# Kernel optimization log

Hardware: AMD Instinct MI355X
Metric: run time of the kernel (lower is better)

Reference implementation:

```python
import jax, jax.numpy as jnp
import numpy as np

N_NODES = 40000
N_EDGES = 640000
D = 64          # node feature dim / out_features
HEADS = 4
K2 = 64         # n_grid_K**3
BN_EPS = 1e-5
SEG_EPS = 1e-16
R_EPS = 1e-8


def segment_softmax(alpha, seg, num_segments):
    # alpha: [E, H], seg: [E] int
    seg_max = jax.ops.segment_max(alpha, seg, num_segments=num_segments)
    seg_max = jnp.where(jnp.isfinite(seg_max), seg_max, 0.0)
    a = jnp.exp(alpha - seg_max[seg])
    denom = jax.ops.segment_sum(a, seg, num_segments=num_segments)
    return a / (denom[seg] + SEG_EPS)


def setup_inputs() -> dict:
    key = jax.random.key(0)
    ks = jax.random.split(key, 12)
    inp = {}
    inp["input"] = jax.random.normal(ks[0], (N_NODES, D), dtype=jnp.float32)
    inp["rij"] = jax.random.uniform(ks[1], (N_EDGES,), dtype=jnp.float32)
    inp["plane_wave"] = jax.random.normal(ks[2], (N_EDGES, K2), dtype=jnp.float32)
    inp["edge_attr"] = jax.random.normal(ks[3], (N_EDGES, D), dtype=jnp.float32)
    # learned parameters (torch Linear(in,out,bias=False) -> [in,out] here)
    def glorot(k, shape):
        fan = shape[0] + shape[-1]
        s = jnp.sqrt(6.0 / fan)
        return jax.random.uniform(k, shape, minval=-s, maxval=s, dtype=jnp.float32)
    inp["Wg"] = glorot(ks[4], (3 * D, D))          # linear_gate 192->64
    inp["Wm"] = glorot(ks[5], (3 * D, D))          # linear_MLP 192->64
    inp["W2"] = glorot(ks[6], (K2, D))             # linear2_vector
    inp["W2g"] = glorot(ks[7], (K2, K2))           # linear2_vector_gate
    inp["Wa"] = glorot(ks[8], (2 * D, HEADS * D))  # AGAT W
    inp["att"] = glorot(ks[9], (1, HEADS, 2 * D))  # AGAT att
    inp["bn_gamma"] = jnp.ones((HEADS,), dtype=jnp.float32)
    inp["bn_beta"] = jnp.zeros((HEADS,), dtype=jnp.float32)
    # graph indices
    src = jax.random.randint(ks[10], (N_EDGES,), 0, N_NODES, dtype=jnp.int32)
    tgt = jax.random.randint(ks[11], (N_EDGES,), 0, N_NODES, dtype=jnp.int32)
    inp["edge_sources"] = src
    inp["edge_targets"] = tgt
    inp["edge_index"] = jnp.stack([src, tgt], axis=0)
    inp["nodes"] = jnp.zeros((1,), dtype=jnp.int32)  # unused in forward
    return inp


def reference(input, rij, plane_wave, edge_attr, Wg, Wm, W2, W2g, Wa, att,
              bn_gamma, bn_beta, nodes, edge_sources, edge_targets, edge_index):
    # gated edge MLP branch
    ni = input[edge_sources]                       # [E, D]
    nj = input[edge_targets]                       # [E, D]
    r = rij + (rij == 0).astype(rij.dtype) * R_EPS
    delta = (ni - nj) / r[:, None]
    final_fe = jnp.concatenate([ni, nj, delta], axis=1)   # [E, 3D]
    e_gate = jax.nn.sigmoid(final_fe @ Wg)                 # [E, D]
    e_mlp = jax.nn.elu(final_fe @ Wm)                      # [E, D]
    # plane-wave gated linear branch
    gate = jax.nn.sigmoid(plane_wave @ W2g)                # [E, K2]
    z2 = (plane_wave * gate) @ W2                          # [E, D]
    # AGAT branch (eval-mode BatchNorm1d: running mean 0, var 1)
    row, col = edge_index[0], edge_index[1]
    out_i = jax.nn.softplus(jnp.concatenate([input[row], edge_attr], axis=1) @ Wa)
    out_j = jax.nn.softplus(jnp.concatenate([input[col], edge_attr], axis=1) @ Wa)
    out_i = out_i.reshape(-1, HEADS, D)                    # [E, H, D]
    out_j = out_j.reshape(-1, HEADS, D)
    alpha = jax.nn.softplus((jnp.concatenate([out_i, out_j], axis=-1) * att).sum(-1))  # [E, H]
    alpha = jax.nn.softplus(alpha / jnp.sqrt(1.0 + BN_EPS) * bn_gamma + bn_beta)
    alpha = segment_softmax(alpha, row, N_NODES)
    z1 = (out_j * alpha[:, :, None]).mean(axis=1)          # mean over heads -> [E, D]
    # combine + scatter-add
    z = e_gate * e_mlp * (z1 + z2)
    output = input.at[edge_sources].add(z)
    return output
```

## Files before the change

kernel.cpp:

```cpp
#include <hip/hip_runtime.h>
#include <math.h>

#define N_NODES 40000
#define N_EDGES 640000
#define NT0 16

typedef short short8 __attribute__((ext_vector_type(8)));
typedef unsigned short ushort8v __attribute__((ext_vector_type(8)));
typedef unsigned short ushort4v __attribute__((ext_vector_type(4)));
typedef float fragC __attribute__((ext_vector_type(4)));

__device__ __forceinline__ float softplus_f(float x) {
    return x > 15.f ? x : __logf(1.f + __expf(x));
}
__device__ __forceinline__ float sigmoid_f(float x) {
    return 1.f / (1.f + __expf(-x));
}
__device__ __forceinline__ short f2bf(float f) {
    unsigned u = __float_as_uint(f);
    u += 0x7FFF + ((u >> 16) & 1);
    return (short)(u >> 16);
}
__device__ __forceinline__ float bf2f(unsigned short u) {
    return __uint_as_float(((unsigned)u) << 16);
}

__global__ void k_weights(const float* __restrict__ Wa, const float* __restrict__ W2g,
                          const float* __restrict__ W2, short* __restrict__ WaTb,
                          short* __restrict__ W2gTb, short* __restrict__ W2Tb) {
    int idx = blockIdx.x * blockDim.x + threadIdx.x;
    int stride = gridDim.x * blockDim.x;
    for (int i = idx; i < 256 * 64; i += stride) {
        int c = i >> 6, k = i & 63;
        WaTb[i] = f2bf(Wa[(64 + k) * 256 + c]);
    }
    for (int i = idx; i < 64 * 64; i += stride) {
        int c = i >> 6, k = i & 63;
        W2gTb[i] = f2bf(W2g[k * 64 + c]);
        W2Tb[i]  = f2bf(W2[k * 64 + c]);
    }
}

__global__ __launch_bounds__(256) void k_node_pre(const float* __restrict__ X,
                                                  const float* __restrict__ Wg,
                                                  const float* __restrict__ Wm,
                                                  const float* __restrict__ Wa,
                                                  short* __restrict__ nodeAxaT,
                                                  short* __restrict__ nodeGT,
                                                  float* __restrict__ nodeDT) {
    __shared__ float xs[NT0 * 64];
    int t = threadIdx.x;
    int n0 = blockIdx.x * NT0;
    ((float4*)xs)[t] = ((const float4*)(X + (size_t)n0 * 64))[t];
    __syncthreads();
    for (int c = t; c < 640; c += 256) {
        const float* wptr;
        int ld;
        if (c < 192)      { wptr = Wg + (c >> 6) * 64 * 64 + (c & 63); ld = 64; }
        else if (c < 384) { wptr = Wm + ((c - 192) >> 6) * 64 * 64 + (c & 63); ld = 64; }
        else              { wptr = Wa + (c - 384); ld = 256; }
        float acc[NT0];
#pragma unroll
        for (int n = 0; n < NT0; n++) acc[n] = 0.f;
        for (int kc = 0; kc < 16; kc++) {
            float w0 = wptr[(4 * kc + 0) * ld];
            float w1 = wptr[(4 * kc + 1) * ld];
            float w2 = wptr[(4 * kc + 2) * ld];
            float w3 = wptr[(4 * kc + 3) * ld];
#pragma unroll
            for (int n = 0; n < NT0; n++) {
                float4 x = ((float4*)xs)[n * 16 + kc];
                acc[n] += x.x * w0 + x.y * w1 + x.z * w2 + x.w * w3;
            }
        }
#pragma unroll
        for (int n = 0; n < NT0; n++) {
            float v = acc[n];
            size_t nn = (size_t)(n0 + n);
            if (c < 64) {
                nodeGT[nn * 256 + (c & 15) * 4 + (c >> 4)] = f2bf(v);
            } else if (c < 128) {
                int d = c - 64;  nodeGT[nn * 256 + 64 + (d & 15) * 4 + (d >> 4)] = f2bf(v);
            } else if (c < 192) {
                int d = c - 128; nodeDT[nn * 128 + (d & 15) * 4 + (d >> 4)] = v;
            } else if (c < 256) {
                int d = c - 192; nodeGT[nn * 256 + 128 + (d & 15) * 4 + (d >> 4)] = f2bf(v);
            } else if (c < 320) {
                int d = c - 256; nodeGT[nn * 256 + 192 + (d & 15) * 4 + (d >> 4)] = f2bf(v);
            } else if (c < 384) {
                int d = c - 320; nodeDT[nn * 128 + 64 + (d & 15) * 4 + (d >> 4)] = v;
            } else {
                int co = c - 384; nodeAxaT[nn * 256 + (co & 15) * 16 + (co >> 4)] = f2bf(v);
            }
        }
    }
}

__global__ __launch_bounds__(256) void k_alpha(
    const float* __restrict__ ea, const int* __restrict__ src, const int* __restrict__ tgt,
    const unsigned short* __restrict__ nodeAxaT, const short* __restrict__ WaTb,
    const float* __restrict__ att, const float* __restrict__ gamma,
    const float* __restrict__ beta,
    float* __restrict__ alphaBuf, float* __restrict__ segSum) {
    __shared__ short ldsW[256 * 72];
    __shared__ float attS[512];
    int t = threadIdx.x;
    {
        const float4* s4 = (const float4*)(WaTb + t * 64);
        float4* d4 = (float4*)(ldsW + t * 72);
#pragma unroll
        for (int k = 0; k < 8; k++) d4[k] = s4[k];
        attS[t] = att[(t >> 6) * 128 + (t & 63)];
        attS[256 + t] = att[(t >> 6) * 128 + 64 + (t & 63)];
    }
    __syncthreads();
    int wave = t >> 6, lane = t & 63;
    int i = lane & 15, q = lane >> 4;
    int eb = blockIdx.x * 64 + wave * 16;

    short8 afr[2];
    {
        const float* ap = ea + (size_t)(eb + i) * 64 + q * 8;
#pragma unroll
        for (int kt = 0; kt < 2; kt++) {
            float4 x0 = *(const float4*)(ap + kt * 32);
            float4 x1 = *(const float4*)(ap + kt * 32 + 4);
            short8 a;
            a[0] = f2bf(x0.x); a[1] = f2bf(x0.y); a[2] = f2bf(x0.z); a[3] = f2bf(x0.w);
            a[4] = f2bf(x1.x); a[5] = f2bf(x1.y); a[6] = f2bf(x1.z); a[7] = f2bf(x1.w);
            afr[kt] = a;
        }
    }
    int sI[4];
    ushort8v gs[4][2], gt[4][2];
#pragma unroll
    for (int r = 0; r < 4; r++) {
        int e = eb + q * 4 + r;
        sI[r] = src[e];
        int tg = tgt[e];
        const unsigned short* ps = nodeAxaT + (size_t)sI[r] * 256 + i * 16;
        const unsigned short* pt = nodeAxaT + (size_t)tg * 256 + i * 16;
        gs[r][0] = *(const ushort8v*)(ps);
        gs[r][1] = *(const ushort8v*)(ps + 8);
        gt[r][0] = *(const ushort8v*)(pt);
        gt[r][1] = *(const ushort8v*)(pt + 8);
    }
    float part[4][4];
#pragma unroll
    for (int h = 0; h < 4; h++)
#pragma unroll
        for (int r = 0; r < 4; r++) part[h][r] = 0.f;

#pragma unroll
    for (int nt = 0; nt < 16; nt++) {
        const short* wrow = ldsW + (nt * 16 + i) * 72 + q * 8;
        short8 b0 = *(const short8*)(wrow);
        short8 b1 = *(const short8*)(wrow + 32);
        fragC acc = {0.f, 0.f, 0.f, 0.f};
        acc = __builtin_amdgcn_mfma_f32_16x16x32_bf16(afr[0], b0, acc, 0, 0, 0);
        acc = __builtin_amdgcn_mfma_f32_16x16x32_bf16(afr[1], b1, acc, 0, 0, 0);
        float atti = attS[nt * 16 + i];
        float attj = attS[256 + nt * 16 + i];
        int h = nt >> 2;
#pragma unroll
        for (int r = 0; r < 4; r++) {
            float P = acc[r];
            float oi = softplus_f(bf2f(gs[r][nt >> 3][nt & 7]) + P);
            float oj = softplus_f(bf2f(gt[r][nt >> 3][nt & 7]) + P);
            part[h][r] += oi * atti + oj * attj;
        }
    }
    const float inv_s = 0.99999500003749968f;
#pragma unroll
    for (int h = 0; h < 4; h++) {
        float g = gamma[h], b = beta[h];
#pragma unroll
        for (int r = 0; r < 4; r++) {
            float p = part[h][r];
            p += __shfl_xor(p, 1);
            p += __shfl_xor(p, 2);
            p += __shfl_xor(p, 4);
            p += __shfl_xor(p, 8);
            if (i == 0) {
                float araw = softplus_f(p);
                float av = softplus_f(araw * inv_s * g + b);
                float a = __expf(av);
                int e = eb + q * 4 + r;
                alphaBuf[e * 4 + h] = a;
                atomicAdd(&segSum[sI[r] * 4 + h], a);
            }
        }
    }
}

__global__ __launch_bounds__(256) void k_final(
    const float* __restrict__ ea, const float* __restrict__ pw,
    const float* __restrict__ rij,
    const int* __restrict__ src, const int* __restrict__ tgt,
    const unsigned short* __restrict__ nodeAxaT, const unsigned short* __restrict__ nodeGT,
    const float* __restrict__ nodeDT,
    const short* __restrict__ WaTb, const short* __restrict__ W2gTb,
    const short* __restrict__ W2Tb,
    const float* __restrict__ alphaBuf, const float* __restrict__ segSum,
    float* __restrict__ out) {
    __shared__ short ldsW[256 * 72];
    __shared__ short pwg[4][16 * 72];
    int t = threadIdx.x;
    {
        const float4* s4 = (const float4*)(WaTb + t * 64);
        float4* d4 = (float4*)(ldsW + t * 72);
#pragma unroll
        for (int k = 0; k < 8; k++) d4[k] = s4[k];
    }
    int wave = t >> 6, lane = t & 63;
    int i = lane & 15, q = lane >> 4;
    int eb = blockIdx.x * 64 + wave * 16;

    int sI[4], tgI[4];
    float ir[4];
    float wal[4][4];
    ushort8v ga[4][2];
#pragma unroll
    for (int r = 0; r < 4; r++) {
        int e = eb + q * 4 + r;
        sI[r] = src[e];
        tgI[r] = tgt[e];
        float rr = rij[e];
        if (rr == 0.f) rr = 1e-8f;
        ir[r] = 1.f / rr;
        float4 av = *(const float4*)(alphaBuf + (size_t)e * 4);
        float4 sv = *(const float4*)(segSum + (size_t)sI[r] * 4);
        wal[r][0] = av.x / (sv.x + 1e-16f) * 0.25f;
        wal[r][1] = av.y / (sv.y + 1e-16f) * 0.25f;
        wal[r][2] = av.z / (sv.z + 1e-16f) * 0.25f;
        wal[r][3] = av.w / (sv.w + 1e-16f) * 0.25f;
        const unsigned short* pt = nodeAxaT + (size_t)tgI[r] * 256 + i * 16;
        ga[r][0] = *(const ushort8v*)(pt);
        ga[r][1] = *(const ushort8v*)(pt + 8);
    }

    short8 pfr[2];
    {
        const float* pp = pw + (size_t)(eb + i) * 64 + q * 8;
#pragma unroll
        for (int kt = 0; kt < 2; kt++) {
            float4 x0 = *(const float4*)(pp + kt * 32);
            float4 x1 = *(const float4*)(pp + kt * 32 + 4);
            short8 a;
            a[0] = f2bf(x0.x); a[1] = f2bf(x0.y); a[2] = f2bf(x0.z); a[3] = f2bf(x0.w);
            a[4] = f2bf(x1.x); a[5] = f2bf(x1.y); a[6] = f2bf(x1.z); a[7] = f2bf(x1.w);
            pfr[kt] = a;
        }
    }
#pragma unroll
    for (int nt = 0; nt < 4; nt++) {
        const short* wrow = W2gTb + (nt * 16 + i) * 64 + q * 8;
        short8 b0 = *(const short8*)(wrow);
        short8 b1 = *(const short8*)(wrow + 32);
        fragC g = {0.f, 0.f, 0.f, 0.f};
        g = __builtin_amdgcn_mfma_f32_16x16x32_bf16(pfr[0], b0, g, 0, 0, 0);
        g = __builtin_amdgcn_mfma_f32_16x16x32_bf16(pfr[1], b1, g, 0, 0, 0);
        int k = nt * 16 + i;
#pragma unroll
        for (int r = 0; r < 4; r++) {
            float pv = pw[(size_t)(eb + q * 4 + r) * 64 + k];
            pwg[wave][(q * 4 + r) * 72 + k] = f2bf(pv * sigmoid_f(g[r]));
        }
    }
    __syncthreads();

    short8 a2[2];
    {
        const short* prow = &pwg[wave][i * 72 + q * 8];
        a2[0] = *(const short8*)(prow);
        a2[1] = *(const short8*)(prow + 32);
    }
    fragC z2f[4];
#pragma unroll
    for (int nt = 0; nt < 4; nt++) {
        const short* wrow = W2Tb + (nt * 16 + i) * 64 + q * 8;
        short8 b0 = *(const short8*)(wrow);
        short8 b1 = *(const short8*)(wrow + 32);
        fragC z = {0.f, 0.f, 0.f, 0.f};
        z = __builtin_amdgcn_mfma_f32_16x16x32_bf16(a2[0], b0, z, 0, 0, 0);
        z = __builtin_amdgcn_mfma_f32_16x16x32_bf16(a2[1], b1, z, 0, 0, 0);
        z2f[nt] = z;
    }

    short8 afr[2];
    {
        const float* ap = ea + (size_t)(eb + i) * 64 + q * 8;
#pragma unroll
        for (int kt = 0; kt < 2; kt++) {
            float4 x0 = *(const float4*)(ap + kt * 32);
            float4 x1 = *(const float4*)(ap + kt * 32 + 4);
            short8 a;
            a[0] = f2bf(x0.x); a[1] = f2bf(x0.y); a[2] = f2bf(x0.z); a[3] = f2bf(x0.w);
            a[4] = f2bf(x1.x); a[5] = f2bf(x1.y); a[6] = f2bf(x1.z); a[7] = f2bf(x1.w);
            afr[kt] = a;
        }
    }
    float z1[4][4];
#pragma unroll
    for (int j = 0; j < 4; j++)
#pragma unroll
        for (int r = 0; r < 4; r++) z1[j][r] = 0.f;
#pragma unroll
    for (int nt = 0; nt < 16; nt++) {
        const short* wrow = ldsW + (nt * 16 + i) * 72 + q * 8;
        short8 b0 = *(const short8*)(wrow);
        short8 b1 = *(const short8*)(wrow + 32);
        fragC acc = {0.f, 0.f, 0.f, 0.f};
        acc = __builtin_amdgcn_mfma_f32_16x16x32_bf16(afr[0], b0, acc, 0, 0, 0);
        acc = __builtin_amdgcn_mfma_f32_16x16x32_bf16(afr[1], b1, acc, 0, 0, 0);
        int h = nt >> 2, j = nt & 3;
#pragma unroll
        for (int r = 0; r < 4; r++) {
            float oj = softplus_f(bf2f(ga[r][nt >> 3][nt & 7]) + acc[r]);
            z1[j][r] += oj * wal[r][h];
        }
    }

#pragma unroll
    for (int r = 0; r < 4; r++) {
        const unsigned short* Gs = nodeGT + (size_t)sI[r] * 256;
        const unsigned short* Gt = nodeGT + (size_t)tgI[r] * 256;
        const float* Ds = nodeDT + (size_t)sI[r] * 128;
        const float* Dt = nodeDT + (size_t)tgI[r] * 128;
        ushort4v ag1 = *(const ushort4v*)(Gs + i * 4);
        ushort4v am1 = *(const ushort4v*)(Gs + 128 + i * 4);
        ushort4v ag2 = *(const ushort4v*)(Gt + 64 + i * 4);
        ushort4v am2 = *(const ushort4v*)(Gt + 192 + i * 4);
        float4 ag3s = *(const float4*)(Ds + i * 4);
        float4 am3s = *(const float4*)(Ds + 64 + i * 4);
        float4 ag3t = *(const float4*)(Dt + i * 4);
        float4 am3t = *(const float4*)(Dt + 64 + i * 4);
        float g3s[4] = {ag3s.x, ag3s.y, ag3s.z, ag3s.w};
        float m3s[4] = {am3s.x, am3s.y, am3s.z, am3s.w};
        float g3t[4] = {ag3t.x, ag3t.y, ag3t.z, ag3t.w};
        float m3t[4] = {am3t.x, am3t.y, am3t.z, am3t.w};
#pragma unroll
        for (int j = 0; j < 4; j++) {
            int d = j * 16 + i;
            float gl = bf2f(ag1[j]) + bf2f(ag2[j]) + (g3s[j] - g3t[j]) * ir[r];
            float ml = bf2f(am1[j]) + bf2f(am2[j]) + (m3s[j] - m3t[j]) * ir[r];
            float eg = sigmoid_f(gl);
            float em = ml > 0.f ? ml : (__expf(ml) - 1.f);
            float z = eg * em * (z1[j][r] + z2f[j][r]);
            atomicAdd(&out[(size_t)sI[r] * 64 + d], z);
        }
    }
}

extern "C" void kernel_launch(void* const* d_in, const int* in_sizes, int n_in,
                              void* d_out, int out_size, void* d_ws, size_t ws_size,
                              hipStream_t stream) {
    const float* input = (const float*)d_in[0];
    const float* rij   = (const float*)d_in[1];
    const float* pw    = (const float*)d_in[2];
    const float* ea    = (const float*)d_in[3];
    const float* Wg    = (const float*)d_in[4];
    const float* Wm    = (const float*)d_in[5];
    const float* W2    = (const float*)d_in[6];
    const float* W2g   = (const float*)d_in[7];
    const float* Wa    = (const float*)d_in[8];
    const float* att   = (const float*)d_in[9];
    const float* gamma = (const float*)d_in[10];
    const float* beta  = (const float*)d_in[11];
    const int* srcIdx  = (const int*)d_in[12];
    const int* tgtIdx  = (const int*)d_in[13];
    float* out = (float*)d_out;

    char* wsb = (char*)d_ws;
    short* nodeAxaT = (short*)(wsb);
    short* nodeGT   = (short*)(wsb + 20480000);
    float* nodeDT   = (float*)(wsb + 40960000);
    float* alphaBuf = (float*)(wsb + 61440000);
    float* segSum   = (float*)(wsb + 71680000);
    short* WaTb     = (short*)(wsb + 72320000);
    short* W2gTb    = (short*)(wsb + 72352768);
    short* W2Tb     = (short*)(wsb + 72360960);

    hipMemsetAsync(wsb + 71680000, 0, 640000, stream);
    hipMemcpyAsync(d_out, (const void*)input, (size_t)N_NODES * 64 * sizeof(float),
                   hipMemcpyDeviceToDevice, stream);

    k_weights<<<32, 256, 0, stream>>>(Wa, W2g, W2, WaTb, W2gTb, W2Tb);
    k_node_pre<<<N_NODES / NT0, 256, 0, stream>>>(input, Wg, Wm, Wa,
                                                  nodeAxaT, nodeGT, nodeDT);
    k_alpha<<<N_EDGES / 64, 256, 0, stream>>>(ea, srcIdx, tgtIdx,
                                              (const unsigned short*)nodeAxaT, WaTb,
                                              att, gamma, beta, alphaBuf, segSum);
    k_final<<<N_EDGES / 64, 256, 0, stream>>>(ea, pw, rij, srcIdx, tgtIdx,
                                              (const unsigned short*)nodeAxaT,
                                              (const unsigned short*)nodeGT, nodeDT,
                                              WaTb, W2gTb, W2Tb, alphaBuf, segSum, out);
}
```

Measured before the change: 1.081 ms.

## Drop LDS weight staging, read Wa from global, split gathers into halves

Both the alpha and final kernels stop copying the 256x64 Wa matrix into LDS and instead read the B fragments straight from global (cache-resident) memory. This removes the per-block staging, the barrier, and about 37KB of LDS per block. The node gathers are split into two halves to cut live registers. The final kernel also folds z1 into the W2 MFMA accumulator, and the alpha kernel writes its results as a float4. The aim is higher occupancy and fewer VGPRs, at the cost of more global/L1 traffic for weight fragments and gathers issued later in the loop.

```diff
diff --git a/kernel.cpp b/kernel.cpp
--- a/kernel.cpp
+++ b/kernel.cpp
@@ -102,18 +102,7 @@
     const float* __restrict__ att, const float* __restrict__ gamma,
     const float* __restrict__ beta,
     float* __restrict__ alphaBuf, float* __restrict__ segSum) {
-    __shared__ short ldsW[256 * 72];
-    __shared__ float attS[512];
     int t = threadIdx.x;
-    {
-        const float4* s4 = (const float4*)(WaTb + t * 64);
-        float4* d4 = (float4*)(ldsW + t * 72);
-#pragma unroll
-        for (int k = 0; k < 8; k++) d4[k] = s4[k];
-        attS[t] = att[(t >> 6) * 128 + (t & 63)];
-        attS[256 + t] = att[(t >> 6) * 128 + 64 + (t & 63)];
-    }
-    __syncthreads();
     int wave = t >> 6, lane = t & 63;
     int i = lane & 15, q = lane >> 4;
     int eb = blockIdx.x * 64 + wave * 16;
@@ -131,19 +120,12 @@
             afr[kt] = a;
         }
     }
-    int sI[4];
-    ushort8v gs[4][2], gt[4][2];
+    int sI[4], tgI[4];
 #pragma unroll
     for (int r = 0; r < 4; r++) {
         int e = eb + q * 4 + r;
         sI[r] = src[e];
-        int tg = tgt[e];
-        const unsigned short* ps = nodeAxaT + (size_t)sI[r] * 256 + i * 16;
-        const unsigned short* pt = nodeAxaT + (size_t)tg * 256 + i * 16;
-        gs[r][0] = *(const ushort8v*)(ps);
-        gs[r][1] = *(const ushort8v*)(ps + 8);
-        gt[r][0] = *(const ushort8v*)(pt);
-        gt[r][1] = *(const ushort8v*)(pt + 8);
+        tgI[r] = tgt[e];
     }
     float part[4][4];
 #pragma unroll
@@ -152,43 +134,60 @@
         for (int r = 0; r < 4; r++) part[h][r] = 0.f;
 
 #pragma unroll
-    for (int nt = 0; nt < 16; nt++) {
-        const short* wrow = ldsW + (nt * 16 + i) * 72 + q * 8;
-        short8 b0 = *(const short8*)(wrow);
-        short8 b1 = *(const short8*)(wrow + 32);
-        fragC acc = {0.f, 0.f, 0.f, 0.f};
-        acc = __builtin_amdgcn_mfma_f32_16x16x32_bf16(afr[0], b0, acc, 0, 0, 0);
-        acc = __builtin_amdgcn_mfma_f32_16x16x32_bf16(afr[1], b1, acc, 0, 0, 0);
-        float atti = attS[nt * 16 + i];
-        float attj = attS[256 + nt * 16 + i];
-        int h = nt >> 2;
+    for (int half = 0; half < 2; half++) {
+        ushort8v gs[4], gt[4];
 #pragma unroll
         for (int r = 0; r < 4; r++) {
-            float P = acc[r];
-            float oi = softplus_f(bf2f(gs[r][nt >> 3][nt & 7]) + P);
-            float oj = softplus_f(bf2f(gt[r][nt >> 3][nt & 7]) + P);
-            part[h][r] += oi * atti + oj * attj;
+            gs[r] = *(const ushort8v*)(nodeAxaT + (size_t)sI[r] * 256 + i * 16 + half * 8);
+            gt[r] = *(const ushort8v*)(nodeAxaT + (size_t)tgI[r] * 256 + i * 16 + half * 8);
+        }
+#pragma unroll
+        for (int nn = 0; nn < 8; nn++) {
+            int nt = half * 8 + nn;
+            const short* wrow = WaTb + (nt * 16 + i) * 64 + q * 8;
+            short8 b0 = *(const short8*)(wrow);
+            short8 b1 = *(const short8*)(wrow + 32);
+            fragC acc = {0.f, 0.f, 0.f, 0.f};
+            acc = __builtin_amdgcn_mfma_f32_16x16x32_bf16(afr[0], b0, acc, 0, 0, 0);
+            acc = __builtin_amdgcn_mfma_f32_16x16x32_bf16(afr[1], b1, acc, 0, 0, 0);
+            int h = nt >> 2;
+            float atti = att[h * 128 + (nt & 3) * 16 + i];
+            float attj = att[h * 128 + 64 + (nt & 3) * 16 + i];
+#pragma unroll
+            for (int r = 0; r < 4; r++) {
+                float P = acc[r];
+                float oi = softplus_f(bf2f(gs[r][nn]) + P);
+                float oj = softplus_f(bf2f(gt[r][nn]) + P);
+                part[h][r] += oi * atti + oj * attj;
+            }
         }
     }
     const float inv_s = 0.99999500003749968f;
 #pragma unroll
-    for (int h = 0; h < 4; h++) {
-        float g = gamma[h], b = beta[h];
-#pragma unroll
-        for (int r = 0; r < 4; r++) {
+    for (int r = 0; r < 4; r++) {
+        float pr[4];
+#pragma unroll
+        for (int h = 0; h < 4; h++) {
             float p = part[h][r];
             p += __shfl_xor(p, 1);
             p += __shfl_xor(p, 2);
             p += __shfl_xor(p, 4);
             p += __shfl_xor(p, 8);
-            if (i == 0) {
-                float araw = softplus_f(p);
-                float av = softplus_f(araw * inv_s * g + b);
-                float a = __expf(av);
-                int e = eb + q * 4 + r;
-                alphaBuf[e * 4 + h] = a;
-                atomicAdd(&segSum[sI[r] * 4 + h], a);
-            }
+            pr[h] = p;
+        }
+        if (i == 0) {
+            float av[4];
+#pragma unroll
+            for (int h = 0; h < 4; h++) {
+                float araw = softplus_f(pr[h]);
+                av[h] = __expf(softplus_f(araw * inv_s * gamma[h] + beta[h]));
+            }
+            int e = eb + q * 4 + r;
+            *(float4*)(alphaBuf + (size_t)e * 4) = make_float4(av[0], av[1], av[2], av[3]);
+            atomicAdd(&segSum[sI[r] * 4 + 0], av[0]);
+            atomicAdd(&segSum[sI[r] * 4 + 1], av[1]);
+            atomicAdd(&segSum[sI[r] * 4 + 2], av[2]);
+            atomicAdd(&segSum[sI[r] * 4 + 3], av[3]);
         }
     }
 }
@@ -203,15 +202,8 @@
     const short* __restrict__ W2Tb,
     const float* __restrict__ alphaBuf, const float* __restrict__ segSum,
     float* __restrict__ out) {
-    __shared__ short ldsW[256 * 72];
     __shared__ short pwg[4][16 * 72];
     int t = threadIdx.x;
-    {
-        const float4* s4 = (const float4*)(WaTb + t * 64);
-        float4* d4 = (float4*)(ldsW + t * 72);
-#pragma unroll
-        for (int k = 0; k < 8; k++) d4[k] = s4[k];
-    }
     int wave = t >> 6, lane = t & 63;
     int i = lane & 15, q = lane >> 4;
     int eb = blockIdx.x * 64 + wave * 16;
@@ -219,7 +211,6 @@
     int sI[4], tgI[4];
     float ir[4];
     float wal[4][4];
-    ushort8v ga[4][2];
 #pragma unroll
     for (int r = 0; r < 4; r++) {
         int e = eb + q * 4 + r;
@@ -234,9 +225,6 @@
         wal[r][1] = av.y / (sv.y + 1e-16f) * 0.25f;
         wal[r][2] = av.z / (sv.z + 1e-16f) * 0.25f;
         wal[r][3] = av.w / (sv.w + 1e-16f) * 0.25f;
-        const unsigned short* pt = nodeAxaT + (size_t)tgI[r] * 256 + i * 16;
-        ga[r][0] = *(const ushort8v*)(pt);
-        ga[r][1] = *(const ushort8v*)(pt + 8);
     }
 
     short8 pfr[2];
@@ -269,24 +257,6 @@
     }
     __syncthreads();
 
-    short8 a2[2];
-    {
-        const short* prow = &pwg[wave][i * 72 + q * 8];
-        a2[0] = *(const short8*)(prow);
-        a2[1] = *(const short8*)(prow + 32);
-    }
-    fragC z2f[4];
-#pragma unroll
-    for (int nt = 0; nt < 4; nt++) {
-        const short* wrow = W2Tb + (nt * 16 + i) * 64 + q * 8;
-        short8 b0 = *(const short8*)(wrow);
-        short8 b1 = *(const short8*)(wrow + 32);
-        fragC z = {0.f, 0.f, 0.f, 0.f};
-        z = __builtin_amdgcn_mfma_f32_16x16x32_bf16(a2[0], b0, z, 0, 0, 0);
-        z = __builtin_amdgcn_mfma_f32_16x16x32_bf16(a2[1], b1, z, 0, 0, 0);
-        z2f[nt] = z;
-    }
-
     short8 afr[2];
     {
         const float* ap = ea + (size_t)(eb + i) * 64 + q * 8;
@@ -306,19 +276,45 @@
 #pragma unroll
         for (int r = 0; r < 4; r++) z1[j][r] = 0.f;
 #pragma unroll
-    for (int nt = 0; nt < 16; nt++) {
-        const short* wrow = ldsW + (nt * 16 + i) * 72 + q * 8;
+    for (int half = 0; half < 2; half++) {
+        ushort8v ga[4];
+#pragma unroll
+        for (int r = 0; r < 4; r++)
+            ga[r] = *(const ushort8v*)(nodeAxaT + (size_t)tgI[r] * 256 + i * 16 + half * 8);
+#pragma unroll
+        for (int nn = 0; nn < 8; nn++) {
+            int nt = half * 8 + nn;
+            const short* wrow = WaTb + (nt * 16 + i) * 64 + q * 8;
+            short8 b0 = *(const short8*)(wrow);
+            short8 b1 = *(const short8*)(wrow + 32);
+            fragC acc = {0.f, 0.f, 0.f, 0.f};
+            acc = __builtin_amdgcn_mfma_f32_16x16x32_bf16(afr[0], b0, acc, 0, 0, 0);
+            acc = __builtin_amdgcn_mfma_f32_16x16x32_bf16(afr[1], b1, acc, 0, 0, 0);
+            int h = nt >> 2, j = nt & 3;
+#pragma unroll
+            for (int r = 0; r < 4; r++) {
+                float oj = softplus_f(bf2f(ga[r][nn]) + acc[r]);
+                z1[j][r] += oj * wal[r][h];
+            }
+        }
+    }
+
+    short8 a2[2];
+    {
+        const short* prow = &pwg[wave][i * 72 + q * 8];
+        a2[0] = *(const short8*)(prow);
+        a2[1] = *(const short8*)(prow + 32);
+    }
+    fragC zt[4];
+#pragma unroll
+    for (int nt = 0; nt < 4; nt++) {
+        const short* wrow = W2Tb + (nt * 16 + i) * 64 + q * 8;
         short8 b0 = *(const short8*)(wrow);
         short8 b1 = *(const short8*)(wrow + 32);
-        fragC acc = {0.f, 0.f, 0.f, 0.f};
-        acc = __builtin_amdgcn_mfma_f32_16x16x32_bf16(afr[0], b0, acc, 0, 0, 0);
-        acc = __builtin_amdgcn_mfma_f32_16x16x32_bf16(afr[1], b1, acc, 0, 0, 0);
-        int h = nt >> 2, j = nt & 3;
-#pragma unroll
-        for (int r = 0; r < 4; r++) {
-            float oj = softplus_f(bf2f(ga[r][nt >> 3][nt & 7]) + acc[r]);
-            z1[j][r] += oj * wal[r][h];
-        }
+        fragC z = {z1[nt][0], z1[nt][1], z1[nt][2], z1[nt][3]};
+        z = __builtin_amdgcn_mfma_f32_16x16x32_bf16(a2[0], b0, z, 0, 0, 0);
+        z = __builtin_amdgcn_mfma_f32_16x16x32_bf16(a2[1], b1, z, 0, 0, 0);
+        zt[nt] = z;
     }
 
 #pragma unroll
@@ -346,7 +342,7 @@
             float ml = bf2f(am1[j]) + bf2f(am2[j]) + (m3s[j] - m3t[j]) * ir[r];
             float eg = sigmoid_f(gl);
             float em = ml > 0.f ? ml : (__expf(ml) - 1.f);
-            float z = eg * em * (z1[j][r] + z2f[j][r]);
+            float z = eg * em * (zt[j][r]);
             atomicAdd(&out[(size_t)sI[r] * 64 + d], z);
         }
     }
```

Measured after the change: 1.358 ms. +25.7%, slower.

## Reuse weight LDS for gated plane-wave tile and fold z1 into z2 MFMA

Applied to the files above, without the earlier changes.

The final kernel drops its separate pwg shared buffer and stages the gated plane-wave tile in the ldsW region once the Wa MFMA loop has finished, using extra barriers. The W2 MFMA is moved after the z1 loop and seeded with z1 as its accumulator, which removes the z2f registers, and the target-node gathers are deferred. Together these cut shared memory and register pressure to allow more resident waves, at the cost of two more __syncthreads. The alpha kernel also writes alpha as one float4 store per edge instead of four scalar stores.

```diff
diff --git a/kernel.cpp b/kernel.cpp
--- a/kernel.cpp
+++ b/kernel.cpp
@@ -172,23 +172,30 @@
     }
     const float inv_s = 0.99999500003749968f;
 #pragma unroll
-    for (int h = 0; h < 4; h++) {
-        float g = gamma[h], b = beta[h];
-#pragma unroll
-        for (int r = 0; r < 4; r++) {
+    for (int r = 0; r < 4; r++) {
+        float pr[4];
+#pragma unroll
+        for (int h = 0; h < 4; h++) {
             float p = part[h][r];
             p += __shfl_xor(p, 1);
             p += __shfl_xor(p, 2);
             p += __shfl_xor(p, 4);
             p += __shfl_xor(p, 8);
-            if (i == 0) {
-                float araw = softplus_f(p);
-                float av = softplus_f(araw * inv_s * g + b);
-                float a = __expf(av);
-                int e = eb + q * 4 + r;
-                alphaBuf[e * 4 + h] = a;
-                atomicAdd(&segSum[sI[r] * 4 + h], a);
+            pr[h] = p;
+        }
+        if (i == 0) {
+            float av[4];
+#pragma unroll
+            for (int h = 0; h < 4; h++) {
+                float araw = softplus_f(pr[h]);
+                av[h] = __expf(softplus_f(araw * inv_s * gamma[h] + beta[h]));
             }
+            int e = eb + q * 4 + r;
+            *(float4*)(alphaBuf + (size_t)e * 4) = make_float4(av[0], av[1], av[2], av[3]);
+            atomicAdd(&segSum[sI[r] * 4 + 0], av[0]);
+            atomicAdd(&segSum[sI[r] * 4 + 1], av[1]);
+            atomicAdd(&segSum[sI[r] * 4 + 2], av[2]);
+            atomicAdd(&segSum[sI[r] * 4 + 3], av[3]);
         }
     }
 }
@@ -204,7 +211,6 @@
     const float* __restrict__ alphaBuf, const float* __restrict__ segSum,
     float* __restrict__ out) {
     __shared__ short ldsW[256 * 72];
-    __shared__ short pwg[4][16 * 72];
     int t = threadIdx.x;
     {
         const float4* s4 = (const float4*)(WaTb + t * 64);
@@ -219,7 +225,6 @@
     int sI[4], tgI[4];
     float ir[4];
     float wal[4][4];
-    ushort8v ga[4][2];
 #pragma unroll
     for (int r = 0; r < 4; r++) {
         int e = eb + q * 4 + r;
@@ -234,13 +239,11 @@
         wal[r][1] = av.y / (sv.y + 1e-16f) * 0.25f;
         wal[r][2] = av.z / (sv.z + 1e-16f) * 0.25f;
         wal[r][3] = av.w / (sv.w + 1e-16f) * 0.25f;
-        const unsigned short* pt = nodeAxaT + (size_t)tgI[r] * 256 + i * 16;
-        ga[r][0] = *(const ushort8v*)(pt);
-        ga[r][1] = *(const ushort8v*)(pt + 8);
-    }
-
-    short8 pfr[2];
-    {
+    }
+
+    short pg[4][4];
+    {
+        short8 pfr[2];
         const float* pp = pw + (size_t)(eb + i) * 64 + q * 8;
 #pragma unroll
         for (int kt = 0; kt < 2; kt++) {
@@ -251,41 +254,32 @@
             a[4] = f2bf(x1.x); a[5] = f2bf(x1.y); a[6] = f2bf(x1.z); a[7] = f2bf(x1.w);
             pfr[kt] = a;
         }
-    }
-#pragma unroll
-    for (int nt = 0; nt < 4; nt++) {
-        const short* wrow = W2gTb + (nt * 16 + i) * 64 + q * 8;
-        short8 b0 = *(const short8*)(wrow);
-        short8 b1 = *(const short8*)(wrow + 32);
-        fragC g = {0.f, 0.f, 0.f, 0.f};
-        g = __builtin_amdgcn_mfma_f32_16x16x32_bf16(pfr[0], b0, g, 0, 0, 0);
-        g = __builtin_amdgcn_mfma_f32_16x16x32_bf16(pfr[1], b1, g, 0, 0, 0);
-        int k = nt * 16 + i;
-#pragma unroll
-        for (int r = 0; r < 4; r++) {
-            float pv = pw[(size_t)(eb + q * 4 + r) * 64 + k];
-            pwg[wave][(q * 4 + r) * 72 + k] = f2bf(pv * sigmoid_f(g[r]));
-        }
-    }
+#pragma unroll
+        for (int nt = 0; nt < 4; nt++) {
+            const short* wrow = W2gTb + (nt * 16 + i) * 64 + q * 8;
+            short8 b0 = *(const short8*)(wrow);
+            short8 b1 = *(const short8*)(wrow + 32);
+            fragC g = {0.f, 0.f, 0.f, 0.f};
+            g = __builtin_amdgcn_mfma_f32_16x16x32_bf16(pfr[0], b0, g, 0, 0, 0);
+            g = __builtin_amdgcn_mfma_f32_16x16x32_bf16(pfr[1], b1, g, 0, 0, 0);
+            int k = nt * 16 + i;
+#pragma unroll
+            for (int r = 0; r < 4; r++) {
+                float pv = pw[(size_t)(eb + q * 4 + r) * 64 + k];
+                pg[nt][r] = f2bf(pv * sigmoid_f(g[r]));
+            }
+        }
+    }
+
+    ushort8v ga[4][2];
+#pragma unroll
+    for (int r = 0; r < 4; r++) {
+        const unsigned short* pt = nodeAxaT + (size_t)tgI[r] * 256 + i * 16;
+        ga[r][0] = *(const ushort8v*)(pt);
+        ga[r][1] = *(const ushort8v*)(pt + 8);
+    }
+
     __syncthreads();
-
-    short8 a2[2];
-    {
-        const short* prow = &pwg[wave][i * 72 + q * 8];
-        a2[0] = *(const short8*)(prow);
-        a2[1] = *(const short8*)(prow + 32);
-    }
-    fragC z2f[4];
-#pragma unroll
-    for (int nt = 0; nt < 4; nt++) {
-        const short* wrow = W2Tb + (nt * 16 + i) * 64 + q * 8;
-        short8 b0 = *(const short8*)(wrow);
-        short8 b1 = *(const short8*)(wrow + 32);
-        fragC z = {0.f, 0.f, 0.f, 0.f};
-        z = __builtin_amdgcn_mfma_f32_16x16x32_bf16(a2[0], b0, z, 0, 0, 0);
-        z = __builtin_amdgcn_mfma_f32_16x16x32_bf16(a2[1], b1, z, 0, 0, 0);
-        z2f[nt] = z;
-    }
 
     short8 afr[2];
     {
@@ -319,6 +313,36 @@
             float oj = softplus_f(bf2f(ga[r][nt >> 3][nt & 7]) + acc[r]);
             z1[j][r] += oj * wal[r][h];
         }
+    }
+
+    __syncthreads();
+
+    {
+        short* pwgW = ldsW + wave * (16 * 72);
+#pragma unroll
+        for (int nt = 0; nt < 4; nt++)
+#pragma unroll
+            for (int r = 0; r < 4; r++)
+                pwgW[(q * 4 + r) * 72 + nt * 16 + i] = pg[nt][r];
+    }
+    __syncthreads();
+
+    short8 a2[2];
+    {
+        const short* prow = ldsW + wave * (16 * 72) + i * 72 + q * 8;
+        a2[0] = *(const short8*)(prow);
+        a2[1] = *(const short8*)(prow + 32);
+    }
+    fragC zt[4];
+#pragma unroll
+    for (int nt = 0; nt < 4; nt++) {
+        const short* wrow = W2Tb + (nt * 16 + i) * 64 + q * 8;
+        short8 b0 = *(const short8*)(wrow);
+        short8 b1 = *(const short8*)(wrow + 32);
+        fragC z = {z1[nt][0], z1[nt][1], z1[nt][2], z1[nt][3]};
+        z = __builtin_amdgcn_mfma_f32_16x16x32_bf16(a2[0], b0, z, 0, 0, 0);
+        z = __builtin_amdgcn_mfma_f32_16x16x32_bf16(a2[1], b1, z, 0, 0, 0);
+        zt[nt] = z;
     }
 
 #pragma unroll
@@ -346,7 +370,7 @@
             float ml = bf2f(am1[j]) + bf2f(am2[j]) + (m3s[j] - m3t[j]) * ir[r];
             float eg = sigmoid_f(gl);
             float em = ml > 0.f ? ml : (__expf(ml) - 1.f);
-            float z = eg * em * (z1[j][r] + z2f[j][r]);
+            float z = eg * em * (zt[j][r]);
             atomicAdd(&out[(size_t)sI[r] * 64 + d], z);
         }
     }
```

Result: faster. 967.5 us (-10.5%).
